# Kernel optimization log

Hardware: AMD Instinct MI355X
Metric: run time of the kernel (lower is better)

## Reference

```python
import jax, jax.numpy as jnp
import numpy as np

B, Q, K, D_TO, D_FROM, H = 16, 2048, 2048, 768, 768, 768

def setup_inputs() -> dict:
    key = jax.random.key(0)
    ks = jax.random.split(key, 8)
    s = 0.02
    return {
        "x_to": jax.random.normal(ks[0], (B, Q, D_TO), jnp.float32),
        "x_from": jax.random.normal(ks[1], (B, K, D_FROM), jnp.float32),
        "Wq": jax.random.normal(ks[2], (D_TO, H), jnp.float32) * s,
        "bq": jnp.zeros((H,), jnp.float32),
        "Wk": jax.random.normal(ks[3], (D_FROM, H), jnp.float32) * s,
        "bk": jnp.zeros((H,), jnp.float32),
        "Wv": jax.random.normal(ks[4], (D_FROM, H), jnp.float32) * s,
        "bv": jnp.zeros((H,), jnp.float32),
    }

def reference(x_to, x_from, Wq, bq, Wk, bk, Wv, bv):
    q = x_to @ Wq + bq          # [b,q,h]
    k = x_from @ Wk + bk        # [b,k,h]
    v = x_from @ Wv + bv        # [b,k,h]
    scores = jnp.einsum('bqd,bkd->bqk', q, k) / jnp.sqrt(jnp.float32(H))
    attn = jax.nn.softmax(scores, axis=-1)
    return jnp.einsum('bqk,bkd->bqd', attn, v)
```

## Files before the change

kernel.cpp:

```cpp
#include <hip/hip_runtime.h>

typedef unsigned short u16;
typedef __attribute__((ext_vector_type(8))) short s16x8;
typedef __attribute__((ext_vector_type(4))) float f32x4;

__device__ __forceinline__ u16 f2bf(float f) {
  unsigned u = __builtin_bit_cast(unsigned, f);
  return (u16)((u + 0x7fffu + ((u >> 16) & 1u)) >> 16);
}
__device__ __forceinline__ float bf2f(u16 h) {
  return __builtin_bit_cast(float, (unsigned)h << 16);
}

#define GLOAD16(gp, lp) __builtin_amdgcn_global_load_lds( \
    (__attribute__((address_space(1))) void*)(gp),        \
    (__attribute__((address_space(3))) void*)(lp), 16, 0, 0)

template<bool OUT_F32>
__global__ __launch_bounds__(256, 3) void gemm_bt(
    const u16* __restrict__ A, int lda, long sA,
    const u16* __restrict__ Bt, int ldb, long sB,
    void* __restrict__ Cv, int ldc, long sC,
    const float* __restrict__ bias, int biasMode, float scale, int K)
{
  __shared__ u16 lsA[128 * 32];
  __shared__ u16 lsB[128 * 32];

  const int t = threadIdx.x;
  const int wave = t >> 6, lane = t & 63;
  const long brow = (long)blockIdx.x * 128;
  const long bcol = (long)blockIdx.y * 128;
  const int z = blockIdx.z;
  A  += z * sA;
  Bt += z * sB;

  const int srow = t >> 2;
  const int skb  = (t & 3) * 16;
  const char* gA0 = (const char*)(A  + (brow + srow)      * (long)lda) + skb;
  const char* gA1 = (const char*)(A  + (brow + 64 + srow) * (long)lda) + skb;
  const char* gB0 = (const char*)(Bt + (bcol + srow)      * (long)ldb) + skb;
  const char* gB1 = (const char*)(Bt + (bcol + 64 + srow) * (long)ldb) + skb;
  u16* lA0 = &lsA[(wave * 64) * 8];
  u16* lA1 = &lsA[(256 + wave * 64) * 8];
  u16* lB0 = &lsB[(wave * 64) * 8];
  u16* lB1 = &lsB[(256 + wave * 64) * 8];

  const int wr = (wave >> 1) * 64;
  const int wc = (wave & 1) * 64;
  const int ar = lane & 15;
  const int ak = (lane >> 4) * 8;

  f32x4 acc[4][4];
  #pragma unroll
  for (int i = 0; i < 4; ++i)
    #pragma unroll
    for (int j = 0; j < 4; ++j)
      acc[i][j] = (f32x4){0.f, 0.f, 0.f, 0.f};

  for (int k0 = 0; k0 < K; k0 += 32) {
    GLOAD16(gA0, lA0);
    GLOAD16(gA1, lA1);
    GLOAD16(gB0, lB0);
    GLOAD16(gB1, lB1);
    gA0 += 64; gA1 += 64; gB0 += 64; gB1 += 64;
    __syncthreads();

    s16x8 a[4], b[4];
    #pragma unroll
    for (int m = 0; m < 4; ++m)
      a[m] = *(const s16x8*)&lsA[(wr + m * 16 + ar) * 32 + ak];
    #pragma unroll
    for (int n = 0; n < 4; ++n)
      b[n] = *(const s16x8*)&lsB[(wc + n * 16 + ar) * 32 + ak];
    #pragma unroll
    for (int m = 0; m < 4; ++m)
      #pragma unroll
      for (int n = 0; n < 4; ++n)
        acc[m][n] = __builtin_amdgcn_mfma_f32_16x16x32_bf16(a[m], b[n], acc[m][n], 0, 0, 0);
    __syncthreads();
  }

  const long row0 = brow + wr + (lane >> 4) * 4;
  const long col0 = bcol + wc + (lane & 15);
  #pragma unroll
  for (int m = 0; m < 4; ++m) {
    #pragma unroll
    for (int n = 0; n < 4; ++n) {
      #pragma unroll
      for (int r = 0; r < 4; ++r) {
        long row = row0 + m * 16 + r;
        long col = col0 + n * 16;
        float v = acc[m][n][r] * scale;
        if (biasMode == 1) v += bias[col];
        else if (biasMode == 2) v += bias[row];
        if constexpr (OUT_F32)
          ((float*)Cv)[(long)z * sC + row * (long)ldc + col] = v;
        else
          ((u16*)Cv)[(long)z * sC + row * (long)ldc + col] = f2bf(v);
      }
    }
  }
}

__global__ __launch_bounds__(256) void cvt_x(const float4* __restrict__ in,
                                             u16* __restrict__ out) {
  long i = (long)blockIdx.x * 256 + threadIdx.x;
  float4 v = in[i];
  uint2 o;
  o.x = (unsigned)f2bf(v.x) | ((unsigned)f2bf(v.y) << 16);
  o.y = (unsigned)f2bf(v.z) | ((unsigned)f2bf(v.w) << 16);
  *(uint2*)(out + i * 4) = o;
}

__global__ __launch_bounds__(256) void cvt_trw(const float* __restrict__ W,
                                               u16* __restrict__ WT) {
  int idx = blockIdx.x * 256 + threadIdx.x;
  int h = idx / 768;
  int d = idx - h * 768;
  WT[idx] = f2bf(W[d * 768 + h]);
}

__global__ __launch_bounds__(256) void softmax_rows(u16* __restrict__ S) {
  const int t = threadIdx.x;
  const int wave = t >> 6, lane = t & 63;
  u16* row = S + (long)blockIdx.x * 2048;
  s16x8 v = *(const s16x8*)(row + t * 8);
  float f[8];
  #pragma unroll
  for (int j = 0; j < 8; ++j) f[j] = bf2f((u16)v[j]);
  float mx = f[0];
  #pragma unroll
  for (int j = 1; j < 8; ++j) mx = fmaxf(mx, f[j]);
  #pragma unroll
  for (int off = 32; off > 0; off >>= 1) mx = fmaxf(mx, __shfl_xor(mx, off, 64));
  __shared__ float smax[4];
  __shared__ float ssum[4];
  if (lane == 0) smax[wave] = mx;
  __syncthreads();
  mx = fmaxf(fmaxf(smax[0], smax[1]), fmaxf(smax[2], smax[3]));
  float s = 0.f;
  #pragma unroll
  for (int j = 0; j < 8; ++j) { f[j] = __expf(f[j] - mx); s += f[j]; }
  #pragma unroll
  for (int off = 32; off > 0; off >>= 1) s += __shfl_xor(s, off, 64);
  if (lane == 0) ssum[wave] = s;
  __syncthreads();
  s = (ssum[0] + ssum[1]) + (ssum[2] + ssum[3]);
  float inv = 1.f / s;
  s16x8 o;
  #pragma unroll
  for (int j = 0; j < 8; ++j) o[j] = (short)f2bf(f[j] * inv);
  *(s16x8*)(row + t * 8) = o;
}

extern "C" void kernel_launch(void* const* d_in, const int* in_sizes, int n_in,
                              void* d_out, int out_size, void* d_ws, size_t ws_size,
                              hipStream_t stream) {
  const float* x_to   = (const float*)d_in[0];
  const float* x_from = (const float*)d_in[1];
  const float* Wq = (const float*)d_in[2];
  const float* bq = (const float*)d_in[3];
  const float* Wk = (const float*)d_in[4];
  const float* bk = (const float*)d_in[5];
  const float* Wv = (const float*)d_in[6];
  const float* bv = (const float*)d_in[7];

  const long NX = 16L * 2048 * 768;
  const long NW = 768L * 768;

  u16* Qb  = (u16*)d_ws;
  u16* Kb  = Qb + NX;
  u16* Vt  = Kb + NX;
  u16* reg2 = Vt + NX;
  u16* Sb  = reg2;
  u16* xtb = reg2;
  u16* xfb = xtb + NX;
  u16* WqT = xfb + NX;
  u16* WkT = WqT + NW;
  u16* WvT = WkT + NW;

  cvt_x<<<24576, 256, 0, stream>>>((const float4*)x_to, xtb);
  cvt_x<<<24576, 256, 0, stream>>>((const float4*)x_from, xfb);
  cvt_trw<<<2304, 256, 0, stream>>>(Wq, WqT);
  cvt_trw<<<2304, 256, 0, stream>>>(Wk, WkT);
  cvt_trw<<<2304, 256, 0, stream>>>(Wv, WvT);

  dim3 blk(256);
  gemm_bt<false><<<dim3(256, 6, 1), blk, 0, stream>>>(
      xtb, 768, 0, WqT, 768, 0, Qb, 768, 0, bq, 1, 1.f, 768);
  gemm_bt<false><<<dim3(256, 6, 1), blk, 0, stream>>>(
      xfb, 768, 0, WkT, 768, 0, Kb, 768, 0, bk, 1, 1.f, 768);
  gemm_bt<false><<<dim3(6, 256, 1), blk, 0, stream>>>(
      WvT, 768, 0, xfb, 768, 0, Vt, 32768, 0, bv, 2, 1.f, 768);

  gemm_bt<false><<<dim3(16, 16, 16), blk, 0, stream>>>(
      Qb, 768, 2048L * 768, Kb, 768, 2048L * 768,
      Sb, 2048, 2048L * 2048, nullptr, 0, 0.03608439182435161f, 768);

  softmax_rows<<<32768, 256, 0, stream>>>(Sb);

  gemm_bt<true><<<dim3(16, 6, 16), blk, 0, stream>>>(
      Sb, 2048, 2048L * 2048, Vt, 32768, 2048,
      (float*)d_out, 768, 2048L * 768, nullptr, 0, 1.f, 2048);
}
```

Measured before the change: 806.8 us.

## Replace GEMM with 256x256 double-buffered swizzled-LDS kernel and batch prep launches

```diff
diff --git a/kernel.cpp b/kernel.cpp
--- a/kernel.cpp
+++ b/kernel.cpp
@@ -16,81 +16,138 @@
     (__attribute__((address_space(1))) void*)(gp),        \
     (__attribute__((address_space(3))) void*)(lp), 16, 0, 0)
 
+#define STG(p, ldx, off) do { \
+    GLOAD16(p, ldst + (off)); \
+    GLOAD16(p + 64 * (ldx), ldst + (off) + 8192); \
+    p += 128; } while (0)
+
+#define LD8(off) (*(const s16x8*)(ldsb + (off)))
+
+#define MFMA2(mi, n) \
+    acc[mi][n] = __builtin_amdgcn_mfma_f32_16x16x32_bf16(af[((mi)&3)*2],   bf[(n)*2],   acc[mi][n], 0,0,0); \
+    acc[mi][n] = __builtin_amdgcn_mfma_f32_16x16x32_bf16(af[((mi)&3)*2+1], bf[(n)*2+1], acc[mi][n], 0,0,0);
+
+#define PH_MID() __builtin_amdgcn_s_barrier(); \
+    asm volatile("s_waitcnt lgkmcnt(0)" ::: "memory"); \
+    __builtin_amdgcn_s_setprio(1)
+#define PH_END() __builtin_amdgcn_s_setprio(0)
+
+#define KTILE(BOFF, OOFF, SA1, SB2, VMW) do { \
+  af[0]=LD8((BOFF)+aoff0);      af[1]=LD8((BOFF)+aoff1); \
+  af[2]=LD8((BOFF)+aoff0+2048); af[3]=LD8((BOFF)+aoff1+2048); \
+  af[4]=LD8((BOFF)+aoff0+4096); af[5]=LD8((BOFF)+aoff1+4096); \
+  af[6]=LD8((BOFF)+aoff0+6144); af[7]=LD8((BOFF)+aoff1+6144); \
+  bf[0]=LD8((BOFF)+boff0);      bf[1]=LD8((BOFF)+boff1); \
+  bf[2]=LD8((BOFF)+boff0+2048); bf[3]=LD8((BOFF)+boff1+2048); \
+  if (SA1) STG(pA1, ldab, (OOFF) + 16384); \
+  asm volatile("s_waitcnt lgkmcnt(8)" ::: "memory"); \
+  PH_MID(); \
+  MFMA2(0,0) MFMA2(1,0) MFMA2(2,0) MFMA2(3,0) \
+  MFMA2(0,1) MFMA2(1,1) MFMA2(2,1) MFMA2(3,1) \
+  PH_END(); __builtin_amdgcn_s_barrier(); \
+  bf[4]=LD8((BOFF)+boff0+4096); bf[5]=LD8((BOFF)+boff1+4096); \
+  bf[6]=LD8((BOFF)+boff0+6144); bf[7]=LD8((BOFF)+boff1+6144); \
+  PH_MID(); \
+  MFMA2(0,2) MFMA2(1,2) MFMA2(2,2) MFMA2(3,2) \
+  MFMA2(0,3) MFMA2(1,3) MFMA2(2,3) MFMA2(3,3) \
+  PH_END(); __builtin_amdgcn_s_barrier(); \
+  af[0]=LD8((BOFF)+aoff0+8192);  af[1]=LD8((BOFF)+aoff1+8192); \
+  af[2]=LD8((BOFF)+aoff0+10240); af[3]=LD8((BOFF)+aoff1+10240); \
+  af[4]=LD8((BOFF)+aoff0+12288); af[5]=LD8((BOFF)+aoff1+12288); \
+  af[6]=LD8((BOFF)+aoff0+14336); af[7]=LD8((BOFF)+aoff1+14336); \
+  if (SB2) STG(pB0, ldbb, (BOFF) + 32768); \
+  PH_MID(); \
+  MFMA2(4,0) MFMA2(5,0) MFMA2(6,0) MFMA2(7,0) \
+  MFMA2(4,1) MFMA2(5,1) MFMA2(6,1) MFMA2(7,1) \
+  PH_END(); __builtin_amdgcn_s_barrier(); \
+  if (SB2) { STG(pB1, ldbb, (BOFF) + 49152); STG(pA0, ldab, (BOFF)); } \
+  PH_MID(); \
+  MFMA2(4,2) MFMA2(5,2) MFMA2(6,2) MFMA2(7,2) \
+  MFMA2(4,3) MFMA2(5,3) MFMA2(6,3) MFMA2(7,3) \
+  PH_END(); \
+  VMW; \
+  __builtin_amdgcn_s_barrier(); \
+} while (0)
+
 template<bool OUT_F32>
-__global__ __launch_bounds__(256, 3) void gemm_bt(
+__global__ __launch_bounds__(512, 2) void gemm256(
     const u16* __restrict__ A, int lda, long sA,
     const u16* __restrict__ Bt, int ldb, long sB,
     void* __restrict__ Cv, int ldc, long sC,
-    const float* __restrict__ bias, int biasMode, float scale, int K)
+    const float* __restrict__ bias, long biasStride, int biasMode,
+    float scale, int K)
 {
-  __shared__ u16 lsA[128 * 32];
-  __shared__ u16 lsB[128 * 32];
-
-  const int t = threadIdx.x;
-  const int wave = t >> 6, lane = t & 63;
-  const long brow = (long)blockIdx.x * 128;
-  const long bcol = (long)blockIdx.y * 128;
+  __shared__ __align__(128) char ldsb[131072];
+  const int tid = threadIdx.x;
+  const int w = tid >> 6, l = tid & 63;
+  const int wm = w >> 2, wn = w & 3;
+  const int q = l >> 4, fr = l & 15;
+
+  int bx, by;
+  { int gx = gridDim.x; int nwg = gx * (int)gridDim.y;
+    int id = blockIdx.y * gx + blockIdx.x;
+    int qq = nwg >> 3, r = nwg & 7, xc = id & 7, ix = id >> 3;
+    int swz = (xc < r ? xc * (qq + 1) : r * (qq + 1) + (xc - r) * qq) + ix;
+    bx = swz % gx; by = swz / gx; }
+  const long brow = (long)bx * 256, bcol = (long)by * 256;
   const int z = blockIdx.z;
-  A  += z * sA;
-  Bt += z * sB;
-
-  const int srow = t >> 2;
-  const int skb  = (t & 3) * 16;
-  const char* gA0 = (const char*)(A  + (brow + srow)      * (long)lda) + skb;
-  const char* gA1 = (const char*)(A  + (brow + 64 + srow) * (long)lda) + skb;
-  const char* gB0 = (const char*)(Bt + (bcol + srow)      * (long)ldb) + skb;
-  const char* gB1 = (const char*)(Bt + (bcol + 64 + srow) * (long)ldb) + skb;
-  u16* lA0 = &lsA[(wave * 64) * 8];
-  u16* lA1 = &lsA[(256 + wave * 64) * 8];
-  u16* lB0 = &lsB[(wave * 64) * 8];
-  u16* lB1 = &lsB[(256 + wave * 64) * 8];
-
-  const int wr = (wave >> 1) * 64;
-  const int wc = (wave & 1) * 64;
-  const int ar = lane & 15;
-  const int ak = (lane >> 4) * 8;
-
-  f32x4 acc[4][4];
-  #pragma unroll
-  for (int i = 0; i < 4; ++i)
+  A += (long)z * sA; Bt += (long)z * sB;
+  if (biasMode) bias += (long)z * biasStride;
+
+  const long ldab = (long)lda * 2, ldbb = (long)ldb * 2;
+  const int rih = w * 8 + (l >> 3);
+  const int sl  = ((l & 7) ^ (l >> 3)) * 16;
+  const char* pA0 = (const char*)A  + (brow + rih) * ldab + sl;
+  const char* pA1 = pA0 + 128 * ldab;
+  const char* pB0 = (const char*)Bt + (bcol + rih) * ldbb + sl;
+  const char* pB1 = pB0 + 128 * ldbb;
+  char* ldst = ldsb + w * 1024;
+
+  const int sw = fr & 7;
+  const int arow_o = (wm * 128 + fr) * 128;
+  const int brow_o = (wn * 64 + fr) * 128 + 32768;
+  const int aoff0 = arow_o + ((q)     ^ sw) * 16;
+  const int aoff1 = arow_o + ((4 + q) ^ sw) * 16;
+  const int boff0 = brow_o + ((q)     ^ sw) * 16;
+  const int boff1 = brow_o + ((4 + q) ^ sw) * 16;
+
+  f32x4 acc[8][4];
+  #pragma unroll
+  for (int i = 0; i < 8; ++i)
     #pragma unroll
-    for (int j = 0; j < 4; ++j)
-      acc[i][j] = (f32x4){0.f, 0.f, 0.f, 0.f};
-
-  for (int k0 = 0; k0 < K; k0 += 32) {
-    GLOAD16(gA0, lA0);
-    GLOAD16(gA1, lA1);
-    GLOAD16(gB0, lB0);
-    GLOAD16(gB1, lB1);
-    gA0 += 64; gA1 += 64; gB0 += 64; gB1 += 64;
-    __syncthreads();
-
-    s16x8 a[4], b[4];
-    #pragma unroll
-    for (int m = 0; m < 4; ++m)
-      a[m] = *(const s16x8*)&lsA[(wr + m * 16 + ar) * 32 + ak];
-    #pragma unroll
-    for (int n = 0; n < 4; ++n)
-      b[n] = *(const s16x8*)&lsB[(wc + n * 16 + ar) * 32 + ak];
-    #pragma unroll
-    for (int m = 0; m < 4; ++m)
-      #pragma unroll
-      for (int n = 0; n < 4; ++n)
-        acc[m][n] = __builtin_amdgcn_mfma_f32_16x16x32_bf16(a[m], b[n], acc[m][n], 0, 0, 0);
-    __syncthreads();
+    for (int j = 0; j < 4; ++j) acc[i][j] = (f32x4){0.f, 0.f, 0.f, 0.f};
+  s16x8 af[8], bf[8];
+
+  STG(pA0, ldab, 0);
+  STG(pA1, ldab, 16384);
+  STG(pB0, ldbb, 32768);
+  STG(pB1, ldbb, 49152);
+  asm volatile("s_waitcnt vmcnt(4)" ::: "memory");
+  STG(pB0, ldbb, 65536 + 32768);
+  STG(pB1, ldbb, 65536 + 49152);
+  STG(pA0, ldab, 65536);
+  asm volatile("s_waitcnt vmcnt(6)" ::: "memory");
+  __builtin_amdgcn_s_barrier();
+
+  const int half_iters = (K >> 7) - 1;
+  for (int it = 0; it < half_iters; ++it) {
+    KTILE(0,     65536, 1, 1, asm volatile("s_waitcnt vmcnt(6)" ::: "memory"));
+    KTILE(65536, 0,     1, 1, asm volatile("s_waitcnt vmcnt(6)" ::: "memory"));
   }
-
-  const long row0 = brow + wr + (lane >> 4) * 4;
-  const long col0 = bcol + wc + (lane & 15);
-  #pragma unroll
-  for (int m = 0; m < 4; ++m) {
+  KTILE(0,     65536, 1, 0, asm volatile("s_waitcnt vmcnt(0)" ::: "memory"));
+  KTILE(65536, 0,     0, 0, ((void)0));
+
+  const long row0 = brow + wm * 128 + q * 4;
+  const long col0 = bcol + wn * 64 + fr;
+  #pragma unroll
+  for (int mi = 0; mi < 8; ++mi) {
     #pragma unroll
     for (int n = 0; n < 4; ++n) {
       #pragma unroll
-      for (int r = 0; r < 4; ++r) {
-        long row = row0 + m * 16 + r;
+      for (int rr = 0; rr < 4; ++rr) {
+        long row = row0 + mi * 16 + rr;
         long col = col0 + n * 16;
-        float v = acc[m][n][r] * scale;
+        float v = acc[mi][n][rr] * scale;
         if (biasMode == 1) v += bias[col];
         else if (biasMode == 2) v += bias[row];
         if constexpr (OUT_F32)
@@ -102,22 +159,35 @@
   }
 }
 
-__global__ __launch_bounds__(256) void cvt_x(const float4* __restrict__ in,
-                                             u16* __restrict__ out) {
+__global__ __launch_bounds__(256) void cvt_x2(const float4* __restrict__ xt,
+                                              const float4* __restrict__ xf,
+                                              u16* __restrict__ out, long NX) {
+  const float4* src = blockIdx.y ? xf : xt;
+  u16* dst = out + (long)blockIdx.y * NX;
   long i = (long)blockIdx.x * 256 + threadIdx.x;
-  float4 v = in[i];
+  float4 v = src[i];
   uint2 o;
   o.x = (unsigned)f2bf(v.x) | ((unsigned)f2bf(v.y) << 16);
   o.y = (unsigned)f2bf(v.z) | ((unsigned)f2bf(v.w) << 16);
-  *(uint2*)(out + i * 4) = o;
-}
-
-__global__ __launch_bounds__(256) void cvt_trw(const float* __restrict__ W,
-                                               u16* __restrict__ WT) {
+  *(uint2*)(dst + i * 4) = o;
+}
+
+__global__ __launch_bounds__(256) void cvt_w3(const float* __restrict__ W0,
+                                              const float* __restrict__ W1,
+                                              const float* __restrict__ W2,
+                                              u16* __restrict__ WT) {
+  const float* W = blockIdx.y == 0 ? W0 : (blockIdx.y == 1 ? W1 : W2);
+  u16* dst = WT + (long)blockIdx.y * 589824;
   int idx = blockIdx.x * 256 + threadIdx.x;
-  int h = idx / 768;
-  int d = idx - h * 768;
-  WT[idx] = f2bf(W[d * 768 + h]);
+  int h = idx / 768, d = idx - h * 768;
+  dst[idx] = f2bf(W[d * 768 + h]);
+}
+
+__global__ __launch_bounds__(256) void pack_bias(const float* __restrict__ bq,
+                                                 const float* __restrict__ bk,
+                                                 float* __restrict__ out) {
+  int i = blockIdx.x * 256 + threadIdx.x;
+  out[i] = i < 768 ? bq[i] : bk[i - 768];
 }
 
 __global__ __launch_bounds__(256) void softmax_rows(u16* __restrict__ S) {
@@ -176,30 +246,23 @@
   u16* xtb = reg2;
   u16* xfb = xtb + NX;
   u16* WqT = xfb + NX;
-  u16* WkT = WqT + NW;
-  u16* WvT = WkT + NW;
-
-  cvt_x<<<24576, 256, 0, stream>>>((const float4*)x_to, xtb);
-  cvt_x<<<24576, 256, 0, stream>>>((const float4*)x_from, xfb);
-  cvt_trw<<<2304, 256, 0, stream>>>(Wq, WqT);
-  cvt_trw<<<2304, 256, 0, stream>>>(Wk, WkT);
-  cvt_trw<<<2304, 256, 0, stream>>>(Wv, WvT);
-
-  dim3 blk(256);
-  gemm_bt<false><<<dim3(256, 6, 1), blk, 0, stream>>>(
-      xtb, 768, 0, WqT, 768, 0, Qb, 768, 0, bq, 1, 1.f, 768);
-  gemm_bt<false><<<dim3(256, 6, 1), blk, 0, stream>>>(
-      xfb, 768, 0, WkT, 768, 0, Kb, 768, 0, bk, 1, 1.f, 768);
-  gemm_bt<false><<<dim3(6, 256, 1), blk, 0, stream>>>(
-      WvT, 768, 0, xfb, 768, 0, Vt, 32768, 0, bv, 2, 1.f, 768);
-
-  gemm_bt<false><<<dim3(16, 16, 16), blk, 0, stream>>>(
+  float* bqk = (float*)(WqT + 3 * NW);
+
+  cvt_x2<<<dim3(24576, 2), 256, 0, stream>>>((const float4*)x_to,
+                                             (const float4*)x_from, xtb, NX);
+  cvt_w3<<<dim3(2304, 3), 256, 0, stream>>>(Wq, Wk, Wv, WqT);
+  pack_bias<<<6, 256, 0, stream>>>(bq, bk, bqk);
+
+  dim3 blk(512);
+  gemm256<false><<<dim3(128, 3, 2), blk, 0, stream>>>(
+      xtb, 768, NX, WqT, 768, NW, Qb, 768, NX, bqk, 768, 1, 1.f, 768);
+  gemm256<false><<<dim3(3, 128, 1), blk, 0, stream>>>(
+      WqT + 2 * NW, 768, 0, xfb, 768, 0, Vt, 32768, 0, bv, 0, 2, 1.f, 768);
+  gemm256<false><<<dim3(8, 8, 16), blk, 0, stream>>>(
       Qb, 768, 2048L * 768, Kb, 768, 2048L * 768,
-      Sb, 2048, 2048L * 2048, nullptr, 0, 0.03608439182435161f, 768);
-
+      Sb, 2048, 2048L * 2048, nullptr, 0, 0, 0.036084391824351615f, 768);
   softmax_rows<<<32768, 256, 0, stream>>>(Sb);
-
-  gemm_bt<true><<<dim3(16, 6, 16), blk, 0, stream>>>(
+  gemm256<true><<<dim3(8, 3, 16), blk, 0, stream>>>(
       Sb, 2048, 2048L * 2048, Vt, 32768, 2048,
-      (float*)d_out, 768, 2048L * 768, nullptr, 0, 1.f, 2048);
-}
+      (float*)d_out, 768, 2048L * 768, nullptr, 0, 0, 1.f, 2048);
+}
```

Result: faster. 763.0 us (-5.4%).
